# Optimization experiments

Measured on AMD Instinct MI355X. Metric: run time of the kernel, lower is better.

## Reference

```python
import jax, jax.numpy as jnp
import numpy as np

B, N, IN_DIM, OUT_DIM, K = 2, 8192, 64, 64, 16


def _mk_linear(key, out_d, in_d):
    k1, k2 = jax.random.split(key)
    W = jax.random.normal(k1, (out_d, in_d), dtype=jnp.float32) * 0.02
    b = jax.random.normal(k2, (out_d,), dtype=jnp.float32) * 0.02
    return W, b


def setup_inputs() -> dict:
    key = jax.random.key(0)
    ks = jax.random.split(key, 11)
    points_xyz = jax.random.normal(ks[0], (B, N, 3), dtype=jnp.float32)
    points_features = jax.random.normal(ks[1], (B, N, IN_DIM), dtype=jnp.float32)
    W1, b1 = _mk_linear(ks[2], OUT_DIM, IN_DIM)
    Wphi, bphi = _mk_linear(ks[3], OUT_DIM, OUT_DIM)
    Wpsi, bpsi = _mk_linear(ks[4], OUT_DIM, OUT_DIM)
    Walpha, balpha = _mk_linear(ks[5], OUT_DIM, OUT_DIM)
    Wgamma, bgamma = _mk_linear(ks[6], OUT_DIM, OUT_DIM)
    Wd1, bd1 = _mk_linear(ks[7], OUT_DIM, 3)
    Wd2, bd2 = _mk_linear(ks[8], OUT_DIM, OUT_DIM)
    W2, b2 = _mk_linear(ks[9], IN_DIM, OUT_DIM)
    return {
        "points_xyz": points_xyz, "points_features": points_features, "k": K,
        "W1": W1, "b1": b1, "Wphi": Wphi, "bphi": bphi, "Wpsi": Wpsi, "bpsi": bpsi,
        "Walpha": Walpha, "balpha": balpha, "Wgamma": Wgamma, "bgamma": bgamma,
        "Wd1": Wd1, "bd1": bd1, "Wd2": Wd2, "bd2": bd2, "W2": W2, "b2": b2,
    }


def _gather(points, idx):
    # points: [B, N, C], idx: [B, S, K] -> [B, S, K, C]
    return jax.vmap(lambda p, i: p[i])(points, idx)


def _knn_indices(xyz, k):
    # euclidean distances (as torch.cdist), then k smallest per query point
    sq = jnp.sum(xyz * xyz, axis=-1)  # [B, N]
    d2 = sq[:, :, None] + sq[:, None, :] - 2.0 * jnp.einsum('bnd,bmd->bnm', xyz, xyz)
    dist = jnp.sqrt(jnp.maximum(d2, 0.0))
    _, idx = jax.lax.top_k(-dist, k)  # smallest distances
    return idx  # [B, N, K]


def reference(points_xyz, points_features, k,
              W1, b1, Wphi, bphi, Wpsi, bpsi, Walpha, balpha, Wgamma, bgamma,
              Wd1, bd1, Wd2, bd2, W2, b2):
    idx = _knn_indices(points_xyz, k)                      # [B, N, K]
    neighbours_xyz = _gather(points_xyz, idx)              # [B, N, K, 3]

    f = points_features @ W1.T + b1                        # linear_1: [B, N, D]
    nf = _gather(f, idx)                                   # [B, N, K, D]

    # positional encoding: MLP on (p_i - p_j)
    diff = points_xyz[:, :, None, :] - neighbours_xyz      # [B, N, K, 3]
    delta = jax.nn.relu((diff @ Wd1.T + bd1) @ Wd2.T + bd2)  # [B, N, K, D]

    beta = (f @ Wphi.T + bphi)[:, :, None, :] - (nf @ Wpsi.T + bpsi) + delta
    gamma = beta @ Wgamma.T + bgamma
    rho = jax.nn.softmax(gamma, axis=-1)                   # softmax over channel dim (as in torch code)
    alpha = (nf @ Walpha.T + balpha) + delta
    out = jnp.sum(rho * alpha, axis=2)                     # reduce over K -> [B, N, D]

    out = out @ W2.T + b2 + points_features                # linear_2 + residual
    return (points_xyz, out)
```

## Files before the change

### kernel.cpp

```cpp
#include <hip/hip_runtime.h>

#define NB 2
#define NP 8192
#define D 64
#define KNN 16
#define NBK 256

__global__ void __launch_bounds__(256)
k_foldall(const float* __restrict__ Wg,   const float* __restrict__ bg,
          const float* __restrict__ Wphi, const float* __restrict__ bphi,
          const float* __restrict__ Wpsi, const float* __restrict__ bpsi,
          const float* __restrict__ Wal,  const float* __restrict__ bal,
          const float* __restrict__ W1,   const float* __restrict__ b1,
          const float* __restrict__ Wd1,  const float* __restrict__ bd1,
          const float* __restrict__ Wd2,  const float* __restrict__ bd2,
          float* __restrict__ Af, float* __restrict__ dAv,
          float* __restrict__ Bf, float* __restrict__ dBv,
          float* __restrict__ Cf, float* __restrict__ dCv,
          float* __restrict__ comb)
{
  __shared__ float sT[64 * 65];
  __shared__ float sTb[64];
  __shared__ float4 sWeff[64];
  const int m   = blockIdx.x;
  const int tid = threadIdx.x;

  if (m == 3) {
    if (tid < 64) {
      const int c = tid;
      float wx = 0.f, wy = 0.f, wz = 0.f, be = bd2[c];
      for (int k = 0; k < 64; ++k) {
        float w = Wd2[c*64 + k];
        wx = fmaf(w, Wd1[k*3+0], wx);
        wy = fmaf(w, Wd1[k*3+1], wy);
        wz = fmaf(w, Wd1[k*3+2], wz);
        be = fmaf(w, bd1[k], be);
      }
      sWeff[c] = make_float4(wx, wy, wz, be);
    }
    __syncthreads();
    #pragma unroll
    for (int it = 0; it < 16; ++it) {
      const int e = it*256 + tid;
      const int o = e >> 6, c = e & 63;
      comb[c*68 + 4 + o] = Wg[e];
    }
    if (tid < 64) {
      float4 wf = sWeff[tid];
      comb[tid*68+0] = wf.x; comb[tid*68+1] = wf.y;
      comb[tid*68+2] = wf.z; comb[tid*68+3] = wf.w;
    }
    return;
  }

  const int o = tid >> 2;
  const int q = tid & 3;

  const float* O  = (m == 2) ? Wal : Wg;
  const float* M  = (m == 0) ? Wphi : Wpsi;
  const float* bM = (m == 0) ? bphi : bpsi;

  if (m == 2) {
    for (int cc = 0; cc < 16; ++cc) sT[o*65 + q*16 + cc] = Wal[o*64 + q*16 + cc];
    if (q == 0) sTb[o] = bal[o];
  } else {
    float acc[16];
    #pragma unroll
    for (int cc = 0; cc < 16; ++cc) acc[cc] = 0.f;
    for (int k = 0; k < 64; ++k) {
      float w = O[o*64 + k];
      #pragma unroll
      for (int cc = 0; cc < 16; ++cc) acc[cc] = fmaf(w, M[k*64 + q*16 + cc], acc[cc]);
    }
    for (int cc = 0; cc < 16; ++cc) sT[o*65 + q*16 + cc] = acc[cc];
    if (q == 0) {
      float tb = (m == 0) ? bg[o] : 0.f;
      for (int k = 0; k < 64; ++k) tb = fmaf(O[o*64 + k], bM[k], tb);
      sTb[o] = tb;
    }
  }
  __syncthreads();

  float acc[16];
  #pragma unroll
  for (int cc = 0; cc < 16; ++cc) acc[cc] = 0.f;
  for (int k = 0; k < 64; ++k) {
    float w = sT[o*65 + k];
    #pragma unroll
    for (int cc = 0; cc < 16; ++cc) acc[cc] = fmaf(w, W1[k*64 + q*16 + cc], acc[cc]);
  }
  float* R  = (m == 0) ? Af  : (m == 1) ? Bf  : Cf;
  float* dR = (m == 0) ? dAv : (m == 1) ? dBv : dCv;
  for (int cc = 0; cc < 16; ++cc) R[o*64 + q*16 + cc] = acc[cc];
  if (q == 0) {
    float db = sTb[o];
    for (int k = 0; k < 64; ++k) db = fmaf(sT[o*65 + k], b1[k], db);
    dR[o] = db;
  }
}

__global__ void __launch_bounds__(256, 2)
k_transform3(const float* __restrict__ feat,
             const float* __restrict__ Af, const float* __restrict__ dAv,
             const float* __restrict__ Bf, const float* __restrict__ dBv,
             const float* __restrict__ Cf, const float* __restrict__ dCv,
             float* __restrict__ uA, float* __restrict__ uB, float* __restrict__ uC)
{
  const int tid   = threadIdx.x;
  const int chunk = blockIdx.y;
  const int m     = chunk >> 2;
  const int rb    = (chunk & 3) << 4;
  const float* __restrict__ M  = (m == 0) ? Af  : ((m == 1) ? Bf  : Cf);
  const float* __restrict__ dv = (m == 0) ? dAv : ((m == 1) ? dBv : dCv);
  float* __restrict__ O        = (m == 0) ? uA  : ((m == 1) ? uB  : uC);

  const size_t pt = (size_t)blockIdx.x * 256 + tid;
  const float4* xr = (const float4*)(feat + pt * D);
  float x[64];
  #pragma unroll
  for (int c4 = 0; c4 < 16; ++c4) {
    float4 v = xr[c4];
    x[c4*4+0] = v.x; x[c4*4+1] = v.y; x[c4*4+2] = v.z; x[c4*4+3] = v.w;
  }

  float acc[16];
  #pragma unroll
  for (int r = 0; r < 16; ++r) {
    acc[r] = dv[rb + r];
    const float4* wr = (const float4*)(M + (size_t)(rb + r) * D);
    #pragma unroll
    for (int c4 = 0; c4 < 16; ++c4) {
      float4 w = wr[c4];
      acc[r] = fmaf(w.x, x[c4*4+0], acc[r]);
      acc[r] = fmaf(w.y, x[c4*4+1], acc[r]);
      acc[r] = fmaf(w.z, x[c4*4+2], acc[r]);
      acc[r] = fmaf(w.w, x[c4*4+3], acc[r]);
    }
  }
  float4* op = (float4*)(O + pt * D + rb);
  #pragma unroll
  for (int q = 0; q < 4; ++q)
    op[q] = make_float4(acc[q*4+0], acc[q*4+1], acc[q*4+2], acc[q*4+3]);
}

__global__ void __launch_bounds__(256)
k_buckets(const float* __restrict__ xyz, float4* __restrict__ brange,
          int* __restrict__ bcur)
{
  __shared__ float smn[256], smx[256];
  __shared__ int hcnt[NBK];
  __shared__ float sr[2];
  const int b = blockIdx.x, tid = threadIdx.x;

  float mn = 1e30f, mx = -1e30f;
  for (int i = tid; i < NP; i += 256) {
    float x = xyz[((size_t)b * NP + i) * 3];
    mn = fminf(mn, x); mx = fmaxf(mx, x);
  }
  smn[tid] = mn; smx[tid] = mx; __syncthreads();
  for (int off = 128; off >= 1; off >>= 1) {
    if (tid < off) {
      smn[tid] = fminf(smn[tid], smn[tid+off]);
      smx[tid] = fmaxf(smx[tid], smx[tid+off]);
    }
    __syncthreads();
  }
  if (tid == 0) {
    float xmin = smn[0], xmax = smx[0];
    float wdt = fmaxf((xmax - xmin) / (float)NBK, 1e-20f);
    brange[b] = make_float4(xmin, 1.0f / wdt, wdt, 0.f);
    sr[0] = xmin; sr[1] = 1.0f / wdt;
  }
  hcnt[tid] = 0;
  __syncthreads();

  const float xmin = sr[0], inv = sr[1];
  for (int i = tid; i < NP; i += 256) {
    float x = xyz[((size_t)b * NP + i) * 3];
    int k = min(max((int)((x - xmin) * inv), 0), NBK - 1);
    atomicAdd(&hcnt[k], 1);
  }
  __syncthreads();

  int v = hcnt[tid];
  int acc = v;
  for (int off = 1; off < NBK; off <<= 1) {
    int t = (tid >= off) ? hcnt[tid - off] : 0;
    __syncthreads();
    acc += t; hcnt[tid] = acc;
    __syncthreads();
  }
  bcur[b*NBK + tid] = acc - v;
}

__global__ void __launch_bounds__(256)
k_scatter(const float* __restrict__ xyz, const float4* __restrict__ brange,
          int* __restrict__ bcur, float4* __restrict__ spts, int* __restrict__ ssidx)
{
  const int i = blockIdx.x * 256 + threadIdx.x;
  const int b = i >> 13;
  const float x = xyz[(size_t)i*3+0];
  const float y = xyz[(size_t)i*3+1];
  const float z = xyz[(size_t)i*3+2];
  const float sq = __fadd_rn(__fadd_rn(__fmul_rn(x,x), __fmul_rn(y,y)), __fmul_rn(z,z));
  float4 br = brange[b];
  int k = min(max((int)((x - br.x) * br.y), 0), NBK - 1);
  int pos = atomicAdd(&bcur[b*NBK + k], 1);
  spts [(size_t)b * NP + pos] = make_float4(x, y, z, sq);
  ssidx[(size_t)b * NP + pos] = i & (NP - 1);
}

__global__ void __launch_bounds__(256)
k_knn8(const float4* __restrict__ spts, const int* __restrict__ ssidx,
       const float4* __restrict__ brange, int* __restrict__ knn_idx)
{
  const int qpos = (blockIdx.x * 256 + threadIdx.x) >> 6;
  const int lane = threadIdx.x & 63;
  const int b    = qpos >> 13;
  const int pos  = qpos & (NP - 1);
  const size_t bb = (size_t)b * NP;

  const float4 qp = spts[bb + pos];
  const float xi = qp.x, yi = qp.y, zi = qp.z, sqi = qp.w;
  const int si_q = ssidx[bb + pos];

  const float slack = __fmul_rn(brange[b].z, 1.01f);

  const int p0 = min(max(pos - 32, 0), NP - 64);

  unsigned kds, kidx;
  float thr_d2;

#define THR_REFRESH()                                                                    \
  {                                                                                      \
    float d16 = __uint_as_float((unsigned)__builtin_amdgcn_readlane((int)kds, KNN - 1)); \
    thr_d2 = __fmul_rn(__fmul_rn(d16, d16), 1.000001f);                                  \
  }

#define KPROCS(P, SIV, VALID)                                                            \
  {                                                                                      \
    float dot = __fadd_rn(__fadd_rn(__fmul_rn(xi,(P).x), __fmul_rn(yi,(P).y)),           \
                          __fmul_rn(zi,(P).z));                                          \
    float d2  = __fsub_rn(__fadd_rn(sqi, (P).w), __fmul_rn(2.0f, dot));                  \
    unsigned long long mask = __ballot((VALID) && d2 <= thr_d2);                         \
    if (mask) {                                                                          \
      float ds = __fsqrt_rn(fmaxf(d2, 0.0f));                                            \
      unsigned cds = __float_as_uint(ds);                                                \
      unsigned cidx = (unsigned)(SIV);                                                   \
      bool ins = false;                                                                  \
      do {                                                                               \
        const int src = __ffsll((long long)mask) - 1;                                    \
        mask &= mask - 1;                                                                \
        const unsigned ids  = (unsigned)__builtin_amdgcn_readlane((int)cds,  src);       \
        const unsigned iidx = (unsigned)__builtin_amdgcn_readlane((int)cidx, src);       \
        const bool less = (kds < ids) || ((kds == ids) && (kidx < iidx));                \
        const int pos2 = __popcll(__ballot((lane < KNN) && less));                       \
        if (pos2 < KNN) {                                                                \
          unsigned uds  = __shfl_up(kds,  1, 64);                                        \
          unsigned uidx = __shfl_up(kidx, 1, 64);                                        \
          if (lane < KNN) {                                                              \
            kds  = (lane < pos2) ? kds  : (lane == pos2 ? ids  : uds);                   \
            kidx = (lane < pos2) ? kidx : (lane == pos2 ? iidx : uidx);                  \
          }                                                                              \
          ins = true;                                                                    \
        }                                                                                \
      } while (mask);                                                                    \
      if (ins) THR_REFRESH()                                                             \
    }                                                                                    \
  }

  {
    float4 P = spts[bb + p0 + lane];
    int SI = ssidx[bb + p0 + lane];
    float dot = __fadd_rn(__fadd_rn(__fmul_rn(xi,P.x), __fmul_rn(yi,P.y)), __fmul_rn(zi,P.z));
    float d2  = __fsub_rn(__fadd_rn(sqi, P.w), __fmul_rn(2.0f, dot));
    float ds  = __fsqrt_rn(fmaxf(d2, 0.0f));
    kds  = __float_as_uint(ds);
    kidx = (unsigned)SI;
  }
  #pragma unroll
  for (int k = 2; k <= 64; k <<= 1) {
    #pragma unroll
    for (int jj = k >> 1; jj >= 1; jj >>= 1) {
      unsigned ods  = __shfl_xor(kds,  jj, 64);
      unsigned oidx = __shfl_xor(kidx, jj, 64);
      const bool up    = (lane & k) == 0;
      const bool lower = (lane & jj) == 0;
      const bool takemin = (lower == up);
      const bool oless = (ods < kds) || ((ods == kds) && (oidx < kidx));
      const bool take = (takemin == oless);
      kds  = take ? ods  : kds;
      kidx = take ? oidx : kidx;
    }
  }
  if (lane >= KNN) { kds = 0x7F7FFFFFu; kidx = 0xFFFFu; }
  THR_REFRESH()

  int l = p0 - 1;
  int r = p0 + 64;
  bool goL = (l >= 0), goR = (r < NP);
  #pragma unroll 1
  while (goL || goR) {
    if (goL) {
      float xl = spts[bb + l].x;
      float gap = (xi - xl) - slack;
      if (gap > 0.f && __fmul_rn(gap, gap) > thr_d2 + 1e-3f) {
        goL = false;
      } else {
        const int base = max(l - 63, 0);
        const int cl = base + lane;
        const bool valid = cl <= l;
        float4 P = spts[bb + cl];
        int SI = ssidx[bb + cl];
        KPROCS(P, SI, valid)
        l = base - 1;
        goL = (l >= 0);
      }
    }
    if (goR) {
      float xr = spts[bb + r].x;
      float gap = (xr - xi) - slack;
      if (gap > 0.f && __fmul_rn(gap, gap) > thr_d2 + 1e-3f) {
        goR = false;
      } else {
        const int cl = min(r + lane, NP - 1);
        const bool valid = (r + lane) < NP;
        float4 P = spts[bb + cl];
        int SI = ssidx[bb + cl];
        KPROCS(P, SI, valid)
        r += 64;
        goR = (r < NP);
      }
    }
  }
#undef KPROCS
#undef THR_REFRESH

  if (lane < KNN) knn_idx[((size_t)b * NP + si_q) * KNN + lane] = (int)kidx;
}

__global__ void __launch_bounds__(256, 4)
k_main5(const float* __restrict__ xyz,
        const float* __restrict__ feat,
        const int* __restrict__ knn_idx,
        const float* __restrict__ uA, const float* __restrict__ uB, const float* __restrict__ uC,
        const float* __restrict__ comb,
        const float* __restrict__ W2g, const float* __restrict__ b2g,
        float* __restrict__ out)
{
  __shared__ float sW2[64 * 68];
  __shared__ float sB2[64];
  __shared__ float sY[16 * 68];

  const int tid = threadIdx.x;
  {
    #pragma unroll
    for (int it = 0; it < 16; ++it) {
      const int e = it*256 + tid;
      sW2[(e >> 6)*68 + (e & 63)] = W2g[e];
    }
    if (tid < 64) sB2[tid] = b2g[tid];
  }
  __syncthreads();

  const int lane  = tid & 63;
  const int kslot = lane & 15;
  const int plocal = (tid >> 6) * 4 + (lane >> 4);
  const int point = blockIdx.x * 16 + plocal;
  const int b     = point >> 13;
  const int i     = point & (NP - 1);
  const size_t irow = (size_t)point * D;

  const int j = knn_idx[(size_t)blockIdx.x * 256 + tid];
  const size_t jrow = ((size_t)(b * NP + j)) * D;

  const float* xb = xyz + (size_t)b * NP * 3;
  const float dx = xb[i*3+0] - xb[j*3+0];
  const float dy = xb[i*3+1] - xb[j*3+1];
  const float dz = xb[i*3+2] - xb[j*3+2];

  float gamma[64];
  {
    const float4* ua = (const float4*)(uA + irow);
    const float4* ub = (const float4*)(uB + jrow);
    #pragma unroll
    for (int cc = 0; cc < 16; ++cc) {
      float4 a = ua[cc];
      float4 v = ub[cc];
      gamma[cc*4+0] = a.x - v.x; gamma[cc*4+1] = a.y - v.y;
      gamma[cc*4+2] = a.z - v.z; gamma[cc*4+3] = a.w - v.w;
    }
  }

  #pragma unroll 4
  for (int c = 0; c < 64; ++c) {
    const float4* rec = (const float4*)(comb + c*68);
    float4 wf = rec[0];
    float t = fmaf(wf.z, dz, fmaf(wf.y, dy, fmaf(wf.x, dx, wf.w)));
    float d = fmaxf(t, 0.f);
    #pragma unroll
    for (int o4 = 0; o4 < 16; ++o4) {
      float4 w = rec[1 + o4];
      gamma[o4*4+0] = fmaf(w.x, d, gamma[o4*4+0]);
      gamma[o4*4+1] = fmaf(w.y, d, gamma[o4*4+1]);
      gamma[o4*4+2] = fmaf(w.z, d, gamma[o4*4+2]);
      gamma[o4*4+3] = fmaf(w.w, d, gamma[o4*4+3]);
    }
  }

  float m0 = gamma[0], m1 = gamma[1], m2 = gamma[2], m3 = gamma[3];
  #pragma unroll
  for (int c = 4; c < 64; c += 4) {
    m0 = fmaxf(m0, gamma[c+0]); m1 = fmaxf(m1, gamma[c+1]);
    m2 = fmaxf(m2, gamma[c+2]); m3 = fmaxf(m3, gamma[c+3]);
  }
  const float m = fmaxf(fmaxf(m0, m1), fmaxf(m2, m3));
  float s0 = 0.f, s1 = 0.f, s2 = 0.f, s3 = 0.f;
  #pragma unroll
  for (int c = 0; c < 64; c += 4) {
    gamma[c+0] = __expf(gamma[c+0] - m); s0 += gamma[c+0];
    gamma[c+1] = __expf(gamma[c+1] - m); s1 += gamma[c+1];
    gamma[c+2] = __expf(gamma[c+2] - m); s2 += gamma[c+2];
    gamma[c+3] = __expf(gamma[c+3] - m); s3 += gamma[c+3];
  }
  const float inv = 1.0f / ((s0 + s1) + (s2 + s3));

  {
    const float4* uc = (const float4*)(uC + jrow);
    #pragma unroll
    for (int cc = 0; cc < 16; ++cc) {
      float4 av = uc[cc];
      float avv[4] = {av.x, av.y, av.z, av.w};
      #pragma unroll
      for (int r = 0; r < 4; ++r) {
        const int c = cc*4 + r;
        const float4* rec = (const float4*)(comb + c*68);
        float4 wf = rec[0];
        float t = fmaf(wf.z, dz, fmaf(wf.y, dy, fmaf(wf.x, dx, wf.w)));
        float d = fmaxf(t, 0.f);
        gamma[c] = gamma[c] * inv * (avv[r] + d);
      }
    }
  }

  float t8[32];
  {
    const bool hi = (kslot & 8) != 0;
    #pragma unroll
    for (int i2 = 0; i2 < 32; ++i2) {
      float sendv = hi ? gamma[i2] : gamma[i2+32];
      float keepv = hi ? gamma[i2+32] : gamma[i2];
      t8[i2] = keepv + __shfl_xor(sendv, 8, 64);
    }
  }
  float t4[16];
  {
    const bool hi = (kslot & 4) != 0;
    #pragma unroll
    for (int i2 = 0; i2 < 16; ++i2) {
      float sendv = hi ? t8[i2] : t8[i2+16];
      float keepv = hi ? t8[i2+16] : t8[i2];
      t4[i2] = keepv + __shfl_xor(sendv, 4, 64);
    }
  }
  float t2[8];
  {
    const bool hi = (kslot & 2) != 0;
    #pragma unroll
    for (int i2 = 0; i2 < 8; ++i2) {
      float sendv = hi ? t4[i2] : t4[i2+8];
      float keepv = hi ? t4[i2+8] : t4[i2];
      t2[i2] = keepv + __shfl_xor(sendv, 2, 64);
    }
  }
  float y0, y1, y2, y3;
  {
    const bool hi = (kslot & 1) != 0;
    float s0v = hi ? t2[0] : t2[4];
    float s1v = hi ? t2[1] : t2[5];
    float s2v = hi ? t2[2] : t2[6];
    float s3v = hi ? t2[3] : t2[7];
    float k0 = hi ? t2[4] : t2[0];
    float k1 = hi ? t2[5] : t2[1];
    float k2 = hi ? t2[6] : t2[2];
    float k3 = hi ? t2[7] : t2[3];
    y0 = k0 + __shfl_xor(s0v, 1, 64);
    y1 = k1 + __shfl_xor(s1v, 1, 64);
    y2 = k2 + __shfl_xor(s2v, 1, 64);
    y3 = k3 + __shfl_xor(s3v, 1, 64);
  }

  ((float4*)sY)[plocal * 17 + kslot] = make_float4(y0, y1, y2, y3);
  __syncthreads();
  float y[64];
  {
    const float4* yp = (const float4*)sY + plocal * 17;
    #pragma unroll
    for (int o4 = 0; o4 < 16; ++o4) {
      float4 v = yp[o4];
      y[o4*4+0] = v.x; y[o4*4+1] = v.y; y[o4*4+2] = v.z; y[o4*4+3] = v.w;
    }
  }

  const int oc = kslot * 4;
  float o0 = sB2[oc+0], o1 = sB2[oc+1], o2 = sB2[oc+2], o3 = sB2[oc+3];
  {
    const float4* r0 = (const float4*)(sW2 + (oc+0)*68);
    const float4* r1 = (const float4*)(sW2 + (oc+1)*68);
    const float4* r2 = (const float4*)(sW2 + (oc+2)*68);
    const float4* r3 = (const float4*)(sW2 + (oc+3)*68);
    #pragma unroll
    for (int c4 = 0; c4 < 16; ++c4) {
      float4 w0 = r0[c4], w1 = r1[c4], w2 = r2[c4], w3 = r3[c4];
      o0 = fmaf(w0.x, y[c4*4+0], o0); o0 = fmaf(w0.y, y[c4*4+1], o0);
      o0 = fmaf(w0.z, y[c4*4+2], o0); o0 = fmaf(w0.w, y[c4*4+3], o0);
      o1 = fmaf(w1.x, y[c4*4+0], o1); o1 = fmaf(w1.y, y[c4*4+1], o1);
      o1 = fmaf(w1.z, y[c4*4+2], o1); o1 = fmaf(w1.w, y[c4*4+3], o1);
      o2 = fmaf(w2.x, y[c4*4+0], o2); o2 = fmaf(w2.y, y[c4*4+1], o2);
      o2 = fmaf(w2.z, y[c4*4+2], o2); o2 = fmaf(w2.w, y[c4*4+3], o2);
      o3 = fmaf(w3.x, y[c4*4+0], o3); o3 = fmaf(w3.y, y[c4*4+1], o3);
      o3 = fmaf(w3.z, y[c4*4+2], o3); o3 = fmaf(w3.w, y[c4*4+3], o3);
    }
  }
  float4 fv = ((const float4*)(feat + irow))[kslot];
  ((float4*)(out + irow))[kslot] = make_float4(o0 + fv.x, o1 + fv.y, o2 + fv.z, o3 + fv.w);
}

extern "C" void kernel_launch(void* const* d_in, const int* in_sizes, int n_in,
                              void* d_out, int out_size, void* d_ws, size_t ws_size,
                              hipStream_t stream) {
  const float* xyz  = (const float*)d_in[0];
  const float* feat = (const float*)d_in[1];
  const float* W1   = (const float*)d_in[3];
  const float* b1   = (const float*)d_in[4];
  const float* Wphi = (const float*)d_in[5];
  const float* bphi = (const float*)d_in[6];
  const float* Wpsi = (const float*)d_in[7];
  const float* bpsi = (const float*)d_in[8];
  const float* Wal  = (const float*)d_in[9];
  const float* bal  = (const float*)d_in[10];
  const float* Wg   = (const float*)d_in[11];
  const float* bg   = (const float*)d_in[12];
  const float* Wd1  = (const float*)d_in[13];
  const float* bd1  = (const float*)d_in[14];
  const float* Wd2  = (const float*)d_in[15];
  const float* bd2  = (const float*)d_in[16];
  const float* W2   = (const float*)d_in[17];
  const float* b2   = (const float*)d_in[18];

  float* out = (float*)d_out;

  const size_t NPT = (size_t)NB * NP;
  float* uA = (float*)d_ws;
  float* uB = uA + NPT * D;
  float* uC = uB + NPT * D;
  int* knn_idx = (int*)(uC + NPT * D);
  float* Af  = (float*)(knn_idx + NPT * KNN);
  float* dAv = Af + 4096;
  float* Bf  = dAv + 64;
  float* dBv = Bf + 4096;
  float* Cf  = dBv + 64;
  float* dCv = Cf + 4096;
  float* comb = dCv + 64;
  int* bcur   = (int*)(comb + 64*68);
  float4* brange = (float4*)(bcur + NB*NBK);
  float4* spts   = brange + 4;
  int* ssidx     = (int*)(spts + NPT);

  hipMemcpyAsync(d_out, d_in[0], NPT * 3 * sizeof(float),
                 hipMemcpyDeviceToDevice, stream);

  k_foldall<<<4, 256, 0, stream>>>(Wg, bg, Wphi, bphi, Wpsi, bpsi, Wal, bal, W1, b1,
                                   Wd1, bd1, Wd2, bd2,
                                   Af, dAv, Bf, dBv, Cf, dCv, comb);
  k_buckets<<<NB, 256, 0, stream>>>(xyz, brange, bcur);
  k_transform3<<<dim3(64, 12), 256, 0, stream>>>(feat, Af, dAv, Bf, dBv, Cf, dCv,
                                                 uA, uB, uC);
  k_scatter<<<NPT / 256, 256, 0, stream>>>(xyz, brange, bcur, spts, ssidx);
  k_knn8<<<NPT / 4, 256, 0, stream>>>(spts, ssidx, brange, knn_idx);
  k_main5<<<NPT / 16, 256, 0, stream>>>(xyz, feat, knn_idx, uA, uB, uC, comb,
                                        W2, b2, out + NPT * 3);
}
```

Before: 224.8 us.

## Store per-point projections in spatially sorted order to improve neighbor gather locality

The scatter kernel now also records each point's position in the x-bucket-sorted order, and the transform kernel writes the uA/uB/uC projections in that sorted order. The main kernel processes points in sorted order and maps each neighbor index through the rank array, so neighbor rows gathered from uA/uB/uC and xyz lie close together in memory. The goal is better cache hit rates on the random K-neighbor gathers. The cost is an extra rank array, one more indirection per neighbor, and scattered reads of features in the transform kernel and of feat/out in the epilogue.

```diff
diff --git a/kernel.cpp b/kernel.cpp
--- a/kernel.cpp
+++ b/kernel.cpp
@@ -99,8 +99,78 @@
   }
 }
 
+__global__ void __launch_bounds__(256)
+k_buckets(const float* __restrict__ xyz, float4* __restrict__ brange,
+          int* __restrict__ bcur)
+{
+  __shared__ float smn[256], smx[256];
+  __shared__ int hcnt[NBK];
+  __shared__ float sr[2];
+  const int b = blockIdx.x, tid = threadIdx.x;
+
+  float mn = 1e30f, mx = -1e30f;
+  for (int i = tid; i < NP; i += 256) {
+    float x = xyz[((size_t)b * NP + i) * 3];
+    mn = fminf(mn, x); mx = fmaxf(mx, x);
+  }
+  smn[tid] = mn; smx[tid] = mx; __syncthreads();
+  for (int off = 128; off >= 1; off >>= 1) {
+    if (tid < off) {
+      smn[tid] = fminf(smn[tid], smn[tid+off]);
+      smx[tid] = fmaxf(smx[tid], smx[tid+off]);
+    }
+    __syncthreads();
+  }
+  if (tid == 0) {
+    float xmin = smn[0], xmax = smx[0];
+    float wdt = fmaxf((xmax - xmin) / (float)NBK, 1e-20f);
+    brange[b] = make_float4(xmin, 1.0f / wdt, wdt, 0.f);
+    sr[0] = xmin; sr[1] = 1.0f / wdt;
+  }
+  hcnt[tid] = 0;
+  __syncthreads();
+
+  const float xmin = sr[0], inv = sr[1];
+  for (int i = tid; i < NP; i += 256) {
+    float x = xyz[((size_t)b * NP + i) * 3];
+    int k = min(max((int)((x - xmin) * inv), 0), NBK - 1);
+    atomicAdd(&hcnt[k], 1);
+  }
+  __syncthreads();
+
+  int v = hcnt[tid];
+  int acc = v;
+  for (int off = 1; off < NBK; off <<= 1) {
+    int t = (tid >= off) ? hcnt[tid - off] : 0;
+    __syncthreads();
+    acc += t; hcnt[tid] = acc;
+    __syncthreads();
+  }
+  bcur[b*NBK + tid] = acc - v;
+}
+
+__global__ void __launch_bounds__(256)
+k_scatter(const float* __restrict__ xyz, const float4* __restrict__ brange,
+          int* __restrict__ bcur, float4* __restrict__ spts, int* __restrict__ ssidx,
+          int* __restrict__ rank)
+{
+  const int i = blockIdx.x * 256 + threadIdx.x;
+  const int b = i >> 13;
+  const int orig = i & (NP - 1);
+  const float x = xyz[(size_t)i*3+0];
+  const float y = xyz[(size_t)i*3+1];
+  const float z = xyz[(size_t)i*3+2];
+  const float sq = __fadd_rn(__fadd_rn(__fmul_rn(x,x), __fmul_rn(y,y)), __fmul_rn(z,z));
+  float4 br = brange[b];
+  int k = min(max((int)((x - br.x) * br.y), 0), NBK - 1);
+  int pos = atomicAdd(&bcur[b*NBK + k], 1);
+  spts [(size_t)b * NP + pos] = make_float4(x, y, z, sq);
+  ssidx[(size_t)b * NP + pos] = orig;
+  rank [(size_t)b * NP + orig] = pos;
+}
+
 __global__ void __launch_bounds__(256, 2)
-k_transform3(const float* __restrict__ feat,
+k_transform4(const float* __restrict__ feat, const int* __restrict__ ssidx,
              const float* __restrict__ Af, const float* __restrict__ dAv,
              const float* __restrict__ Bf, const float* __restrict__ dBv,
              const float* __restrict__ Cf, const float* __restrict__ dCv,
@@ -114,8 +184,12 @@
   const float* __restrict__ dv = (m == 0) ? dAv : ((m == 1) ? dBv : dCv);
   float* __restrict__ O        = (m == 0) ? uA  : ((m == 1) ? uB  : uC);
 
-  const size_t pt = (size_t)blockIdx.x * 256 + tid;
-  const float4* xr = (const float4*)(feat + pt * D);
+  const size_t p = (size_t)blockIdx.x * 256 + tid;
+  const int b = (int)(p >> 13);
+  const int orig = ssidx[p];
+  const size_t frow = ((size_t)(b << 13) + orig) * D;
+
+  const float4* xr = (const float4*)(feat + frow);
   float x[64];
   #pragma unroll
   for (int c4 = 0; c4 < 16; ++c4) {
@@ -137,77 +211,10 @@
       acc[r] = fmaf(w.w, x[c4*4+3], acc[r]);
     }
   }
-  float4* op = (float4*)(O + pt * D + rb);
+  float4* op = (float4*)(O + p * D + rb);
   #pragma unroll
   for (int q = 0; q < 4; ++q)
     op[q] = make_float4(acc[q*4+0], acc[q*4+1], acc[q*4+2], acc[q*4+3]);
-}
-
-__global__ void __launch_bounds__(256)
-k_buckets(const float* __restrict__ xyz, float4* __restrict__ brange,
-          int* __restrict__ bcur)
-{
-  __shared__ float smn[256], smx[256];
-  __shared__ int hcnt[NBK];
-  __shared__ float sr[2];
-  const int b = blockIdx.x, tid = threadIdx.x;
-
-  float mn = 1e30f, mx = -1e30f;
-  for (int i = tid; i < NP; i += 256) {
-    float x = xyz[((size_t)b * NP + i) * 3];
-    mn = fminf(mn, x); mx = fmaxf(mx, x);
-  }
-  smn[tid] = mn; smx[tid] = mx; __syncthreads();
-  for (int off = 128; off >= 1; off >>= 1) {
-    if (tid < off) {
-      smn[tid] = fminf(smn[tid], smn[tid+off]);
-      smx[tid] = fmaxf(smx[tid], smx[tid+off]);
-    }
-    __syncthreads();
-  }
-  if (tid == 0) {
-    float xmin = smn[0], xmax = smx[0];
-    float wdt = fmaxf((xmax - xmin) / (float)NBK, 1e-20f);
-    brange[b] = make_float4(xmin, 1.0f / wdt, wdt, 0.f);
-    sr[0] = xmin; sr[1] = 1.0f / wdt;
-  }
-  hcnt[tid] = 0;
-  __syncthreads();
-
-  const float xmin = sr[0], inv = sr[1];
-  for (int i = tid; i < NP; i += 256) {
-    float x = xyz[((size_t)b * NP + i) * 3];
-    int k = min(max((int)((x - xmin) * inv), 0), NBK - 1);
-    atomicAdd(&hcnt[k], 1);
-  }
-  __syncthreads();
-
-  int v = hcnt[tid];
-  int acc = v;
-  for (int off = 1; off < NBK; off <<= 1) {
-    int t = (tid >= off) ? hcnt[tid - off] : 0;
-    __syncthreads();
-    acc += t; hcnt[tid] = acc;
-    __syncthreads();
-  }
-  bcur[b*NBK + tid] = acc - v;
-}
-
-__global__ void __launch_bounds__(256)
-k_scatter(const float* __restrict__ xyz, const float4* __restrict__ brange,
-          int* __restrict__ bcur, float4* __restrict__ spts, int* __restrict__ ssidx)
-{
-  const int i = blockIdx.x * 256 + threadIdx.x;
-  const int b = i >> 13;
-  const float x = xyz[(size_t)i*3+0];
-  const float y = xyz[(size_t)i*3+1];
-  const float z = xyz[(size_t)i*3+2];
-  const float sq = __fadd_rn(__fadd_rn(__fmul_rn(x,x), __fmul_rn(y,y)), __fmul_rn(z,z));
-  float4 br = brange[b];
-  int k = min(max((int)((x - br.x) * br.y), 0), NBK - 1);
-  int pos = atomicAdd(&bcur[b*NBK + k], 1);
-  spts [(size_t)b * NP + pos] = make_float4(x, y, z, sq);
-  ssidx[(size_t)b * NP + pos] = i & (NP - 1);
 }
 
 __global__ void __launch_bounds__(256)
@@ -340,7 +347,8 @@
 }
 
 __global__ void __launch_bounds__(256, 4)
-k_main5(const float* __restrict__ xyz,
+k_main7(const float4* __restrict__ spts, const int* __restrict__ ssidx,
+        const int* __restrict__ rank,
         const float* __restrict__ feat,
         const int* __restrict__ knn_idx,
         const float* __restrict__ uA, const float* __restrict__ uB, const float* __restrict__ uC,
@@ -366,18 +374,23 @@
   const int lane  = tid & 63;
   const int kslot = lane & 15;
   const int plocal = (tid >> 6) * 4 + (lane >> 4);
-  const int point = blockIdx.x * 16 + plocal;
-  const int b     = point >> 13;
-  const int i     = point & (NP - 1);
-  const size_t irow = (size_t)point * D;
-
-  const int j = knn_idx[(size_t)blockIdx.x * 256 + tid];
-  const size_t jrow = ((size_t)(b * NP + j)) * D;
-
-  const float* xb = xyz + (size_t)b * NP * 3;
-  const float dx = xb[i*3+0] - xb[j*3+0];
-  const float dy = xb[i*3+1] - xb[j*3+1];
-  const float dz = xb[i*3+2] - xb[j*3+2];
+  const int p_s   = blockIdx.x * 16 + plocal;
+  const int b     = p_s >> 13;
+  const size_t bb = (size_t)b * NP;
+
+  const int orig_i = ssidx[p_s];
+  const size_t orow = (bb + (size_t)orig_i) * D;
+  const size_t irow = (size_t)p_s * D;
+
+  const int j = knn_idx[(bb + (size_t)orig_i) * KNN + kslot];
+  const int jpos = rank[bb + (size_t)j];
+  const size_t jrow = (bb + (size_t)jpos) * D;
+
+  const float4 pi = spts[p_s];
+  const float4 pj = spts[bb + (size_t)jpos];
+  const float dx = pi.x - pj.x;
+  const float dy = pi.y - pj.y;
+  const float dz = pi.z - pj.z;
 
   float gamma[64];
   {
@@ -522,8 +535,8 @@
       o3 = fmaf(w3.z, y[c4*4+2], o3); o3 = fmaf(w3.w, y[c4*4+3], o3);
     }
   }
-  float4 fv = ((const float4*)(feat + irow))[kslot];
-  ((float4*)(out + irow))[kslot] = make_float4(o0 + fv.x, o1 + fv.y, o2 + fv.z, o3 + fv.w);
+  float4 fv = ((const float4*)(feat + orow))[kslot];
+  ((float4*)(out + orow))[kslot] = make_float4(o0 + fv.x, o1 + fv.y, o2 + fv.z, o3 + fv.w);
 }
 
 extern "C" void kernel_launch(void* const* d_in, const int* in_sizes, int n_in,
@@ -566,6 +579,7 @@
   float4* brange = (float4*)(bcur + NB*NBK);
   float4* spts   = brange + 4;
   int* ssidx     = (int*)(spts + NPT);
+  int* rank      = ssidx + NPT;
 
   hipMemcpyAsync(d_out, d_in[0], NPT * 3 * sizeof(float),
                  hipMemcpyDeviceToDevice, stream);
@@ -574,10 +588,10 @@
                                    Wd1, bd1, Wd2, bd2,
                                    Af, dAv, Bf, dBv, Cf, dCv, comb);
   k_buckets<<<NB, 256, 0, stream>>>(xyz, brange, bcur);
-  k_transform3<<<dim3(64, 12), 256, 0, stream>>>(feat, Af, dAv, Bf, dBv, Cf, dCv,
+  k_scatter<<<NPT / 256, 256, 0, stream>>>(xyz, brange, bcur, spts, ssidx, rank);
+  k_transform4<<<dim3(64, 12), 256, 0, stream>>>(feat, ssidx, Af, dAv, Bf, dBv, Cf, dCv,
                                                  uA, uB, uC);
-  k_scatter<<<NPT / 256, 256, 0, stream>>>(xyz, brange, bcur, spts, ssidx);
   k_knn8<<<NPT / 4, 256, 0, stream>>>(spts, ssidx, brange, knn_idx);
-  k_main5<<<NPT / 16, 256, 0, stream>>>(xyz, feat, knn_idx, uA, uB, uC, comb,
-                                        W2, b2, out + NPT * 3);
-}
+  k_main7<<<NPT / 16, 256, 0, stream>>>(spts, ssidx, rank, feat, knn_idx,
+                                        uA, uB, uC, comb, W2, b2, out + NPT * 3);
+}
```

New measurement: 223.2 us. No clear change (-0.7%).
